# Kernel tuning notes

Measured on AMD Instinct MI355X. Metric: run time of the kernel, lower is better.

## Reference

```python
import jax, jax.numpy as jnp
import numpy as np

B = 8388608  # batch

def setup_inputs() -> dict:
    key = jax.random.key(0)
    ks = jax.random.split(key, 7)
    x = jax.random.normal(ks[0], (B, 2), dtype=jnp.float32)
    # PyTorch Linear: y = x @ W.T + b, W shape [out, in]
    W1 = jax.random.normal(ks[1], (3, 2), dtype=jnp.float32) * 0.5
    b1 = jax.random.normal(ks[2], (3,), dtype=jnp.float32) * 0.1
    W2 = jax.random.normal(ks[3], (2, 3), dtype=jnp.float32) * 0.5
    b2 = jax.random.normal(ks[4], (2,), dtype=jnp.float32) * 0.1
    W3 = jax.random.normal(ks[5], (1, 2), dtype=jnp.float32) * 0.5
    b3 = jax.random.normal(ks[6], (1,), dtype=jnp.float32) * 0.1
    return {"x": x, "W1": W1, "b1": b1, "W2": W2, "b2": b2, "W3": W3, "b3": b3}

def reference(x, W1, b1, W2, b2, W3, b3):
    h1 = jax.nn.relu(x @ W1.T + b1)          # [B, 3]
    h2 = jax.nn.relu(h1 @ W2.T + b2)         # [B, 2]
    out = jax.nn.sigmoid((h2 @ W3.T + b3).squeeze(-1))  # [B]
    return (out, h1, h2)
```

## Files before the change

kernel.cpp:

```cpp
#include <hip/hip_runtime.h>
#include <math.h>


#define RPB 1024

typedef float v4f __attribute__((ext_vector_type(4)));

__global__ __launch_bounds__(256) void mlp321_kernel(
    const float* __restrict__ x,
    const float* __restrict__ W1, const float* __restrict__ b1,
    const float* __restrict__ W2, const float* __restrict__ b2,
    const float* __restrict__ W3, const float* __restrict__ b3,
    float* __restrict__ out_p, float* __restrict__ h1_p, float* __restrict__ h2_p,
    int nrows)
{
    __shared__ __align__(16) float s_h1[RPB * 3];
    __shared__ __align__(16) float s_h2[RPB * 2];
    __shared__ __align__(16) float s_out[RPB];

    const int tid = threadIdx.x;
    const size_t base = (size_t)blockIdx.x * RPB;

    float w1[6], w2[6], w3v[2], bb1[3], bb2[2], bb3;
#pragma unroll
    for (int i = 0; i < 6; ++i) w1[i] = W1[i];
#pragma unroll
    for (int i = 0; i < 3; ++i) bb1[i] = b1[i];
#pragma unroll
    for (int i = 0; i < 6; ++i) w2[i] = W2[i];
#pragma unroll
    for (int i = 0; i < 2; ++i) bb2[i] = b2[i];
    w3v[0] = W3[0]; w3v[1] = W3[1];
    bb3 = b3[0];

    const bool full = (base + RPB) <= (size_t)nrows;

    const v4f* xv = reinterpret_cast<const v4f*>(x + base * 2);
#pragma unroll
    for (int it = 0; it < 2; ++it) {
        const int idx = it * 256 + tid;
        const int r0 = idx * 2;
        if (!full && (base + r0) >= (size_t)nrows) continue;
        v4f xa = xv[idx];
        float xr[2][2] = {{xa.x, xa.y}, {xa.z, xa.w}};
#pragma unroll
        for (int r = 0; r < 2; ++r) {
            const int row = r0 + r;
            if (!full && (base + row) >= (size_t)nrows) continue;
            const float x0 = xr[r][0], x1 = xr[r][1];
            float h1v[3];
#pragma unroll
            for (int j = 0; j < 3; ++j) {
                float v = fmaf(x0, w1[j * 2 + 0], fmaf(x1, w1[j * 2 + 1], bb1[j]));
                h1v[j] = v > 0.f ? v : 0.f;
                s_h1[row * 3 + j] = h1v[j];
            }
            float h2v[2];
#pragma unroll
            for (int k = 0; k < 2; ++k) {
                float v = bb2[k];
#pragma unroll
                for (int j = 0; j < 3; ++j) v = fmaf(h1v[j], w2[k * 3 + j], v);
                h2v[k] = v > 0.f ? v : 0.f;
                s_h2[row * 2 + k] = h2v[k];
            }
            float z = fmaf(h2v[0], w3v[0], fmaf(h2v[1], w3v[1], bb3));
            s_out[row] = 1.f / (1.f + __expf(-z));
        }
    }
    __syncthreads();

    if (full) {
        const v4f* so = reinterpret_cast<const v4f*>(s_out);
        const v4f* s1 = reinterpret_cast<const v4f*>(s_h1);
        const v4f* s2 = reinterpret_cast<const v4f*>(s_h2);
        v4f* po = reinterpret_cast<v4f*>(out_p + base);
        v4f* p1 = reinterpret_cast<v4f*>(h1_p + base * 3);
        v4f* p2 = reinterpret_cast<v4f*>(h2_p + base * 2);

        __builtin_nontemporal_store(so[tid], po + tid);
#pragma unroll
        for (int it = 0; it < 3; ++it) {
            const int i = it * 256 + tid;
            __builtin_nontemporal_store(s1[i], p1 + i);
        }
#pragma unroll
        for (int it = 0; it < 2; ++it) {
            const int i = it * 256 + tid;
            __builtin_nontemporal_store(s2[i], p2 + i);
        }
    } else {
        const int remain = (int)((size_t)nrows - base);
        for (int r = tid; r < remain; r += 256) {
            out_p[base + r] = s_out[r];
            h1_p[(base + r) * 3 + 0] = s_h1[r * 3 + 0];
            h1_p[(base + r) * 3 + 1] = s_h1[r * 3 + 1];
            h1_p[(base + r) * 3 + 2] = s_h1[r * 3 + 2];
            h2_p[(base + r) * 2 + 0] = s_h2[r * 2 + 0];
            h2_p[(base + r) * 2 + 1] = s_h2[r * 2 + 1];
        }
    }
}

extern "C" void kernel_launch(void* const* d_in, const int* in_sizes, int n_in,
                              void* d_out, int out_size, void* d_ws, size_t ws_size,
                              hipStream_t stream) {
    const float* x  = (const float*)d_in[0];
    const float* W1 = (const float*)d_in[1];
    const float* b1 = (const float*)d_in[2];
    const float* W2 = (const float*)d_in[3];
    const float* b2 = (const float*)d_in[4];
    const float* W3 = (const float*)d_in[5];
    const float* b3 = (const float*)d_in[6];

    const int B = in_sizes[0] / 2;
    float* out_p = (float*)d_out;
    float* h1_p  = out_p + (size_t)B;
    float* h2_p  = h1_p + (size_t)B * 3;

    const int blocks = (B + RPB - 1) / RPB;
    mlp321_kernel<<<blocks, 256, 0, stream>>>(x, W1, b1, W2, b2, W3, b3,
                                              out_p, h1_p, h2_p, B);
}
```

Baseline: 258.5 us.

## Halve rows per block, vectorize LDS staging, use plain stores and fast reciprocal

Reduces rows per block to 512 so each thread handles one float4 of input, and writes LDS with vector stores. Replaces nontemporal global stores with regular stores and splits the leftover output chunk across thread halves. Uses the hardware reciprocal in the sigmoid, and has the tail block write directly to global memory. Aims for higher occupancy and fewer instructions, but trades away the nontemporal cache hint and some sigmoid accuracy.

Result: no change. 259.7 us (+0.4%).

```diff
diff --git a/kernel.cpp b/kernel.cpp
--- a/kernel.cpp
+++ b/kernel.cpp
@@ -2,9 +2,10 @@
 #include <math.h>
 
 
-#define RPB 1024
+#define RPB 512
 
 typedef float v4f __attribute__((ext_vector_type(4)));
+typedef float v2f __attribute__((ext_vector_type(2)));
 
 __global__ __launch_bounds__(256) void mlp321_kernel(
     const float* __restrict__ x,
@@ -35,25 +36,65 @@
 
     const bool full = (base + RPB) <= (size_t)nrows;
 
-    const v4f* xv = reinterpret_cast<const v4f*>(x + base * 2);
-#pragma unroll
-    for (int it = 0; it < 2; ++it) {
-        const int idx = it * 256 + tid;
-        const int r0 = idx * 2;
-        if (!full && (base + r0) >= (size_t)nrows) continue;
-        v4f xa = xv[idx];
-        float xr[2][2] = {{xa.x, xa.y}, {xa.z, xa.w}};
+    if (full) {
+        const v4f* xv = reinterpret_cast<const v4f*>(x + base * 2);
+        v4f xa = xv[tid];
+        const float xr[2][2] = {{xa.x, xa.y}, {xa.z, xa.w}};
+        float h1v[2][3], h2v[2][2], ov[2];
 #pragma unroll
         for (int r = 0; r < 2; ++r) {
-            const int row = r0 + r;
-            if (!full && (base + row) >= (size_t)nrows) continue;
             const float x0 = xr[r][0], x1 = xr[r][1];
+#pragma unroll
+            for (int j = 0; j < 3; ++j) {
+                float v = fmaf(x0, w1[j * 2 + 0], fmaf(x1, w1[j * 2 + 1], bb1[j]));
+                h1v[r][j] = v > 0.f ? v : 0.f;
+            }
+#pragma unroll
+            for (int k = 0; k < 2; ++k) {
+                float v = bb2[k];
+#pragma unroll
+                for (int j = 0; j < 3; ++j) v = fmaf(h1v[r][j], w2[k * 3 + j], v);
+                h2v[r][k] = v > 0.f ? v : 0.f;
+            }
+            const float z = fmaf(h2v[r][0], w3v[0], fmaf(h2v[r][1], w3v[1], bb3));
+            ov[r] = __builtin_amdgcn_rcpf(1.f + __expf(-z));
+        }
+
+        v2f* h1w = reinterpret_cast<v2f*>(&s_h1[6 * tid]);
+        h1w[0] = (v2f){h1v[0][0], h1v[0][1]};
+        h1w[1] = (v2f){h1v[0][2], h1v[1][0]};
+        h1w[2] = (v2f){h1v[1][1], h1v[1][2]};
+        *reinterpret_cast<v4f*>(&s_h2[4 * tid]) =
+            (v4f){h2v[0][0], h2v[0][1], h2v[1][0], h2v[1][1]};
+        *reinterpret_cast<v2f*>(&s_out[2 * tid]) = (v2f){ov[0], ov[1]};
+
+        __syncthreads();
+
+        const v4f* so = reinterpret_cast<const v4f*>(s_out);
+        const v4f* s1 = reinterpret_cast<const v4f*>(s_h1);
+        const v4f* s2 = reinterpret_cast<const v4f*>(s_h2);
+        v4f* po = reinterpret_cast<v4f*>(out_p + base);
+        v4f* p1 = reinterpret_cast<v4f*>(h1_p + base * 3);
+        v4f* p2 = reinterpret_cast<v4f*>(h2_p + base * 2);
+
+        p1[tid] = s1[tid];
+        p2[tid] = s2[tid];
+        if (tid < 128) {
+            p1[256 + tid] = s1[256 + tid];
+        } else {
+            po[tid - 128] = so[tid - 128];
+        }
+    } else {
+        const int remain = (int)((size_t)nrows - base);
+        for (int r = tid; r < remain; r += 256) {
+            const size_t row = base + r;
+            const float x0 = x[row * 2 + 0], x1 = x[row * 2 + 1];
             float h1v[3];
 #pragma unroll
             for (int j = 0; j < 3; ++j) {
                 float v = fmaf(x0, w1[j * 2 + 0], fmaf(x1, w1[j * 2 + 1], bb1[j]));
                 h1v[j] = v > 0.f ? v : 0.f;
-                s_h1[row * 3 + j] = h1v[j];
+                h1_p[row * 3 + j] = h1v[j];
             }
             float h2v[2];
 #pragma unroll
@@ -62,42 +103,10 @@
 #pragma unroll
                 for (int j = 0; j < 3; ++j) v = fmaf(h1v[j], w2[k * 3 + j], v);
                 h2v[k] = v > 0.f ? v : 0.f;
-                s_h2[row * 2 + k] = h2v[k];
+                h2_p[row * 2 + k] = h2v[k];
             }
-            float z = fmaf(h2v[0], w3v[0], fmaf(h2v[1], w3v[1], bb3));
-            s_out[row] = 1.f / (1.f + __expf(-z));
-        }
-    }
-    __syncthreads();
-
-    if (full) {
-        const v4f* so = reinterpret_cast<const v4f*>(s_out);
-        const v4f* s1 = reinterpret_cast<const v4f*>(s_h1);
-        const v4f* s2 = reinterpret_cast<const v4f*>(s_h2);
-        v4f* po = reinterpret_cast<v4f*>(out_p + base);
-        v4f* p1 = reinterpret_cast<v4f*>(h1_p + base * 3);
-        v4f* p2 = reinterpret_cast<v4f*>(h2_p + base * 2);
-
-        __builtin_nontemporal_store(so[tid], po + tid);
-#pragma unroll
-        for (int it = 0; it < 3; ++it) {
-            const int i = it * 256 + tid;
-            __builtin_nontemporal_store(s1[i], p1 + i);
-        }
-#pragma unroll
-        for (int it = 0; it < 2; ++it) {
-            const int i = it * 256 + tid;
-            __builtin_nontemporal_store(s2[i], p2 + i);
-        }
-    } else {
-        const int remain = (int)((size_t)nrows - base);
-        for (int r = tid; r < remain; r += 256) {
-            out_p[base + r] = s_out[r];
-            h1_p[(base + r) * 3 + 0] = s_h1[r * 3 + 0];
-            h1_p[(base + r) * 3 + 1] = s_h1[r * 3 + 1];
-            h1_p[(base + r) * 3 + 2] = s_h1[r * 3 + 2];
-            h2_p[(base + r) * 2 + 0] = s_h2[r * 2 + 0];
-            h2_p[(base + r) * 2 + 1] = s_h2[r * 2 + 1];
+            const float z = fmaf(h2v[0], w3v[0], fmaf(h2v[1], w3v[1], bb3));
+            out_p[row] = __builtin_amdgcn_rcpf(1.f + __expf(-z));
         }
     }
 }
```
